# Optimization experiments

Measured on AMD Instinct MI355X. Metric: run time of the kernel, lower is better.

The kernel has to match this reference:

```python
import jax, jax.numpy as jnp
import numpy as np

HEADS = 8
DIM_HEAD = 64
QUERY_DIM = 512
CONTEXT_DIM = 768
INNER = HEADS * DIM_HEAD  # 512
SCALE = DIM_HEAD ** -0.5


def setup_inputs() -> dict:
    key = jax.random.key(0)
    ks = jax.random.split(key, 7)
    B, N, M = 4, 2048, 2048
    x = jax.random.normal(ks[0], (B, N, QUERY_DIM), dtype=jnp.float32)
    context = jax.random.normal(ks[1], (B, M, CONTEXT_DIM), dtype=jnp.float32)
    # torch Linear weights: [out_features, in_features], y = x @ W.T
    s = 0.02
    Wq = jax.random.normal(ks[2], (INNER, QUERY_DIM), dtype=jnp.float32) * s
    Wk = jax.random.normal(ks[3], (INNER, CONTEXT_DIM), dtype=jnp.float32) * s
    Wv = jax.random.normal(ks[4], (INNER, CONTEXT_DIM), dtype=jnp.float32) * s
    Wo = jax.random.normal(ks[5], (QUERY_DIM, INNER), dtype=jnp.float32) * s
    bo = jax.random.normal(ks[6], (QUERY_DIM,), dtype=jnp.float32) * s
    return {"x": x, "context": context, "Wq": Wq, "Wk": Wk, "Wv": Wv, "Wo": Wo, "bo": bo}


def reference(x, context, Wq, Wk, Wv, Wo, bo):
    b, n, _ = x.shape
    m = context.shape[1]
    h, d = HEADS, DIM_HEAD
    # Projections (bias=False for q/k/v)
    q = jnp.einsum('bnc,ec->bne', x, Wq)        # [b, n, inner]
    k = jnp.einsum('bmc,ec->bme', context, Wk)  # [b, m, inner]
    v = jnp.einsum('bmc,ec->bme', context, Wv)
    # Split heads
    q = q.reshape(b, n, h, d)
    k = k.reshape(b, m, h, d)
    v = v.reshape(b, m, h, d)
    # Scores in fp32 (original casts q,k to float), scaled by dim_head**-0.5
    sim = jnp.einsum('bihd,bjhd->bhij', q.astype(jnp.float32), k.astype(jnp.float32)) * SCALE
    attn = jax.nn.softmax(sim, axis=-1).astype(v.dtype)
    out = jnp.einsum('bhij,bjhd->bihd', attn, v).reshape(b, n, h * d)
    # Output projection with bias (dropout=0 -> identity)
    return jnp.einsum('bne,oe->bno', out, Wo) + bo
```

## Files before the change

kernel.cpp:

```cpp
#include <hip/hip_runtime.h>
#include <hip/hip_bf16.h>
#include <math.h>


typedef __bf16 bf16x8 __attribute__((ext_vector_type(8)));
typedef __bf16 bf16x4 __attribute__((ext_vector_type(4)));
typedef float f32x4 __attribute__((ext_vector_type(4)));

#define QSCALE 0.18033688011112042f

#if __has_builtin(__builtin_amdgcn_exp2f)
#define EXP2(x) __builtin_amdgcn_exp2f(x)
#else
#define EXP2(x) exp2f(x)
#endif

__device__ __forceinline__ f32x4 mfma32(bf16x8 a, bf16x8 b, f32x4 c) {
  return __builtin_amdgcn_mfma_f32_16x16x32_bf16(a, b, c, 0, 0, 0);
}

__global__ __launch_bounds__(256) void cast_all(
    const float* __restrict__ x, const float* __restrict__ ctx,
    const float* __restrict__ wq, const float* __restrict__ wk,
    const float* __restrict__ wv, const float* __restrict__ wo,
    __bf16* __restrict__ xb, __bf16* __restrict__ cb,
    __bf16* __restrict__ wqb, __bf16* __restrict__ wkb,
    __bf16* __restrict__ wvb, __bf16* __restrict__ wob) {
  const int B0 = 1048576;
  const int B1 = 2621440;
  const int B2 = 2686976;
  const int B3 = 2785280;
  const int B4 = 2883584;
  const int B5 = 2949120;
  for (int i = blockIdx.x * blockDim.x + threadIdx.x; i < B5;
       i += gridDim.x * blockDim.x) {
    const float* s;
    __bf16* d;
    int off;
    if (i < B0)      { s = x;   d = xb;  off = i; }
    else if (i < B1) { s = ctx; d = cb;  off = i - B0; }
    else if (i < B2) { s = wq;  d = wqb; off = i - B1; }
    else if (i < B3) { s = wk;  d = wkb; off = i - B2; }
    else if (i < B4) { s = wv;  d = wvb; off = i - B3; }
    else             { s = wo;  d = wob; off = i - B4; }
    float4 f = ((const float4*)s)[off];
    union { __bf16 b[4]; ushort4 u; } cv;
    cv.b[0] = (__bf16)f.x; cv.b[1] = (__bf16)f.y;
    cv.b[2] = (__bf16)f.z; cv.b[3] = (__bf16)f.w;
    ((ushort4*)d)[off] = cv.u;
  }
}

template <int MODE>
__device__ __forceinline__ void gemm_body(
    const __bf16* __restrict__ A, const __bf16* __restrict__ W,
    __bf16* __restrict__ Cout, int Kd, float scale, int m0, int n0,
    __bf16 (*As)[72], __bf16 (*Bs)[72]) {
  const int t = threadIdx.x;
  const int w = t >> 6;
  const int lane = t & 63;
  const int ln = lane & 15;
  const int qd = lane >> 4;
  const int wm = (w >> 1) * 64;
  const int wn = (w & 1) * 64;

  f32x4 zero4 = {0.f, 0.f, 0.f, 0.f};
  f32x4 acc[4][4];
#pragma unroll
  for (int i = 0; i < 4; ++i)
#pragma unroll
    for (int j = 0; j < 4; ++j) acc[i][j] = zero4;

  const int r0 = t >> 2;
  const int c0 = (t & 3) * 16;
  const __bf16* gA0 = A + (size_t)(m0 + r0) * Kd + c0;
  const __bf16* gA1 = A + (size_t)(m0 + r0 + 64) * Kd + c0;
  const __bf16* gB0 = W + (size_t)(n0 + r0) * Kd + c0;
  const __bf16* gB1 = W + (size_t)(n0 + r0 + 64) * Kd + c0;

  uint4 a00 = *(const uint4*)gA0, a01 = *(const uint4*)(gA0 + 8);
  uint4 a10 = *(const uint4*)gA1, a11 = *(const uint4*)(gA1 + 8);
  uint4 b00 = *(const uint4*)gB0, b01 = *(const uint4*)(gB0 + 8);
  uint4 b10 = *(const uint4*)gB1, b11 = *(const uint4*)(gB1 + 8);

  for (int kc = 0; kc < Kd; kc += 64) {
    __syncthreads();
    *(uint4*)&As[r0][c0] = a00;       *(uint4*)&As[r0][c0 + 8] = a01;
    *(uint4*)&As[r0 + 64][c0] = a10;  *(uint4*)&As[r0 + 64][c0 + 8] = a11;
    *(uint4*)&Bs[r0][c0] = b00;       *(uint4*)&Bs[r0][c0 + 8] = b01;
    *(uint4*)&Bs[r0 + 64][c0] = b10;  *(uint4*)&Bs[r0 + 64][c0 + 8] = b11;
    __syncthreads();
    if (kc + 64 < Kd) {
      a00 = *(const uint4*)(gA0 + kc + 64);
      a01 = *(const uint4*)(gA0 + kc + 72);
      a10 = *(const uint4*)(gA1 + kc + 64);
      a11 = *(const uint4*)(gA1 + kc + 72);
      b00 = *(const uint4*)(gB0 + kc + 64);
      b01 = *(const uint4*)(gB0 + kc + 72);
      b10 = *(const uint4*)(gB1 + kc + 64);
      b11 = *(const uint4*)(gB1 + kc + 72);
    }
#pragma unroll
    for (int kst = 0; kst < 2; ++kst) {
      bf16x8 af[4], bfr[4];
#pragma unroll
      for (int i = 0; i < 4; ++i) {
        af[i] = *(const bf16x8*)&As[wm + i * 16 + ln][kst * 32 + qd * 8];
        bfr[i] = *(const bf16x8*)&Bs[wn + i * 16 + ln][kst * 32 + qd * 8];
      }
#pragma unroll
      for (int i = 0; i < 4; ++i)
#pragma unroll
        for (int j = 0; j < 4; ++j) {
          if (MODE == 1)
            acc[i][j] = mfma32(af[i], bfr[j], acc[i][j]);
          else
            acc[i][j] = mfma32(bfr[j], af[i], acc[i][j]);
        }
    }
  }

#pragma unroll
  for (int i = 0; i < 4; ++i)
#pragma unroll
    for (int j = 0; j < 4; ++j) {
      if (MODE == 0) {
        const int gm = m0 + wm + i * 16 + ln;
        const int gn0 = n0 + wn + j * 16 + qd * 4;
        const int bb = gm >> 11, tok = gm & 2047;
        const int hh = gn0 >> 6, dd0 = gn0 & 63;
        bf16x4 v;
#pragma unroll
        for (int rg = 0; rg < 4; ++rg) v[rg] = (__bf16)(acc[i][j][rg] * scale);
        *(bf16x4*)(Cout + (((size_t)bb * 8 + hh) * 2048 + tok) * 64 + dd0) = v;
      } else {
        const int gm0 = m0 + wm + i * 16 + qd * 4;
        const int gn = n0 + wn + j * 16 + ln;
        const int bb = gm0 >> 11, tok0 = gm0 & 2047;
        const int hh = gn >> 6, dd = gn & 63;
        bf16x4 v;
#pragma unroll
        for (int rg = 0; rg < 4; ++rg) v[rg] = (__bf16)acc[i][j][rg];
        *(bf16x4*)(Cout + (((size_t)bb * 8 + hh) * 64 + dd) * 2048 + tok0) = v;
      }
    }
}

__global__ __launch_bounds__(256, 3) void proj_qkv(
    const __bf16* __restrict__ xb, const __bf16* __restrict__ cb,
    const __bf16* __restrict__ Wq, const __bf16* __restrict__ Wk,
    const __bf16* __restrict__ Wv, __bf16* __restrict__ Qw,
    __bf16* __restrict__ Kw, __bf16* __restrict__ Vtw) {
  __shared__ __align__(16) __bf16 As[128][72];
  __shared__ __align__(16) __bf16 Bs[128][72];
  const int m0 = blockIdx.x * 128;
  const int job = blockIdx.y >> 2;
  const int n0 = (blockIdx.y & 3) * 128;
  if (job == 0)
    gemm_body<0>(xb, Wq, Qw, 512, QSCALE, m0, n0, As, Bs);
  else if (job == 1)
    gemm_body<0>(cb, Wk, Kw, 768, 1.0f, m0, n0, As, Bs);
  else
    gemm_body<1>(cb, Wv, Vtw, 768, 1.0f, m0, n0, As, Bs);
}

__global__ __launch_bounds__(256) void gemm_out(
    const __bf16* __restrict__ O0, const __bf16* __restrict__ O1,
    const float* __restrict__ lbuf,
    const __bf16* __restrict__ B,
    float* __restrict__ C, const float* __restrict__ bias) {
  const int m0 = blockIdx.x * 64;
  const int n0 = blockIdx.y * 128;
  const int t = threadIdx.x;
  const int w = t >> 6;
  const int lane = t & 63;
  const int ln = lane & 15;
  const int qd = lane >> 4;
  const int wm = (w >> 1) * 32;
  const int wn = (w & 1) * 64;

  __shared__ __align__(16) __bf16 As[64][72];
  __shared__ __align__(16) __bf16 Bs[128][72];

  f32x4 zero4 = {0.f, 0.f, 0.f, 0.f};
  f32x4 acc[2][4];
#pragma unroll
  for (int i = 0; i < 2; ++i)
#pragma unroll
    for (int j = 0; j < 4; ++j) acc[i][j] = zero4;

  const int r0 = t >> 2;
  const int c0 = (t & 3) * 16;
  const int gm_s = m0 + r0;
  const int bidx = gm_s >> 11, tok_s = gm_s & 2047;
  const size_t aoff = (size_t)gm_s * 512 + c0;
  const __bf16* gB0 = B + (size_t)(n0 + r0) * 512 + c0;
  const __bf16* gB1 = B + (size_t)(n0 + r0 + 64) * 512 + c0;

  float inv[8];
#pragma unroll
  for (int hh = 0; hh < 8; ++hh) {
    const float l0 = lbuf[((size_t)bidx * 8 + hh) * 2048 + tok_s];
    const float l1 = lbuf[65536 + ((size_t)bidx * 8 + hh) * 2048 + tok_s];
    inv[hh] = 1.0f / (l0 + l1);
  }

  uint4 o00 = *(const uint4*)(O0 + aoff), o01 = *(const uint4*)(O0 + aoff + 8);
  uint4 o10 = *(const uint4*)(O1 + aoff), o11 = *(const uint4*)(O1 + aoff + 8);
  uint4 b00 = *(const uint4*)gB0, b01 = *(const uint4*)(gB0 + 8);
  uint4 b10 = *(const uint4*)gB1, b11 = *(const uint4*)(gB1 + 8);

  for (int kc = 0; kc < 512; kc += 64) {
    const float iv = inv[kc >> 6];
    union { bf16x8 v; uint4 u; } u0, u1, r0v, r1v;
    u0.u = o00; u1.u = o10;
#pragma unroll
    for (int e = 0; e < 8; ++e)
      r0v.v[e] = (__bf16)(((float)u0.v[e] + (float)u1.v[e]) * iv);
    u0.u = o01; u1.u = o11;
#pragma unroll
    for (int e = 0; e < 8; ++e)
      r1v.v[e] = (__bf16)(((float)u0.v[e] + (float)u1.v[e]) * iv);
    __syncthreads();
    *(uint4*)&As[r0][c0] = r0v.u;
    *(uint4*)&As[r0][c0 + 8] = r1v.u;
    *(uint4*)&Bs[r0][c0] = b00;       *(uint4*)&Bs[r0][c0 + 8] = b01;
    *(uint4*)&Bs[r0 + 64][c0] = b10;  *(uint4*)&Bs[r0 + 64][c0 + 8] = b11;
    __syncthreads();
    if (kc + 64 < 512) {
      o00 = *(const uint4*)(O0 + aoff + kc + 64);
      o01 = *(const uint4*)(O0 + aoff + kc + 72);
      o10 = *(const uint4*)(O1 + aoff + kc + 64);
      o11 = *(const uint4*)(O1 + aoff + kc + 72);
      b00 = *(const uint4*)(gB0 + kc + 64);
      b01 = *(const uint4*)(gB0 + kc + 72);
      b10 = *(const uint4*)(gB1 + kc + 64);
      b11 = *(const uint4*)(gB1 + kc + 72);
    }
#pragma unroll
    for (int kst = 0; kst < 2; ++kst) {
      bf16x8 af[2], bfr[4];
#pragma unroll
      for (int i = 0; i < 2; ++i)
        af[i] = *(const bf16x8*)&As[wm + i * 16 + ln][kst * 32 + qd * 8];
#pragma unroll
      for (int j = 0; j < 4; ++j)
        bfr[j] = *(const bf16x8*)&Bs[wn + j * 16 + ln][kst * 32 + qd * 8];
#pragma unroll
      for (int i = 0; i < 2; ++i)
#pragma unroll
        for (int j = 0; j < 4; ++j)
          acc[i][j] = mfma32(bfr[j], af[i], acc[i][j]);
    }
  }

#pragma unroll
  for (int i = 0; i < 2; ++i)
#pragma unroll
    for (int j = 0; j < 4; ++j) {
      const int gm = m0 + wm + i * 16 + ln;
      const int gn0 = n0 + wn + j * 16 + qd * 4;
      f32x4 bi = *(const f32x4*)&bias[gn0];
      f32x4 v = acc[i][j] + bi;
      *(f32x4*)&C[(size_t)gm * 512 + gn0] = v;
    }
}

__global__ __launch_bounds__(256, 4) void attn_kernel(
    const __bf16* __restrict__ Q,
    const __bf16* __restrict__ K,
    const __bf16* __restrict__ Vt,
    __bf16* __restrict__ Oh,
    float* __restrict__ lbuf) {
  const int S = 2048;
  const int qt = blockIdx.x;
  const int bh = blockIdx.y;
  const int sp = blockIdx.z;
  const int b = bh >> 3, h = bh & 7;
  const int t = threadIdx.x;
  const int w = t >> 6;
  const int lane = t & 63;
  const int ln = lane & 15;
  const int qd = lane >> 4;

  __shared__ __align__(16) __bf16 Ks[128][72];
  __shared__ __align__(16) __bf16 Vs[64][136];

  bf16x8 bq[2][2];
  {
    const __bf16* qb =
        Q + ((size_t)bh * S + qt * 128 + w * 32 + ln) * 64 + qd * 8;
#pragma unroll
    for (int mt = 0; mt < 2; ++mt)
#pragma unroll
      for (int kst = 0; kst < 2; ++kst)
        bq[mt][kst] = *(const bf16x8*)(qb + mt * 1024 + kst * 32);
  }

  f32x4 zero4 = {0.f, 0.f, 0.f, 0.f};
  f32x4 o[2][4];
  f32x4 o_l[2];
#pragma unroll
  for (int mt = 0; mt < 2; ++mt) {
#pragma unroll
    for (int i = 0; i < 4; ++i) o[mt][i] = zero4;
    o_l[mt] = zero4;
  }
  bf16x8 ones8;
  {
    union { unsigned short u[8]; bf16x8 v; } U;
#pragma unroll
    for (int e = 0; e < 8; ++e) U.u[e] = 0x3F80;
    ones8 = U.v;
  }

  const int kr = t >> 1, kc = (t & 1) * 32;
  const int krow =
      (kr & ~31) | ((kr & 4) << 2) | (((kr >> 3) & 3) << 2) | (kr & 3);
  const int vd = t >> 2, cV = t & 3;
  const int kt0 = sp * 8;

  for (int kt = kt0; kt < kt0 + 8; ++kt) {
    const uint4* gK =
        (const uint4*)(K + ((size_t)bh * S + kt * 128 + kr) * 64 + kc);
    const uint4* gV =
        (const uint4*)(Vt + ((size_t)bh * 64 + vd) * S + kt * 128 + cV * 32);
    uint4 kv0 = gK[0], kv1 = gK[1], kv2 = gK[2], kv3 = gK[3];
    uint4 vv0 = gV[0], vv1 = gV[1], vv2 = gV[2], vv3 = gV[3];
    __syncthreads();
    {
      uint4* dK = (uint4*)&Ks[krow][kc];
      dK[0] = kv0; dK[1] = kv1; dK[2] = kv2; dK[3] = kv3;
      uint4* dV = (uint4*)&Vs[vd][cV * 32];
      dV[0] = vv0; dV[1] = vv1; dV[2] = vv2; dV[3] = vv3;
    }
    __syncthreads();

#pragma unroll
    for (int c = 0; c < 4; ++c) {
      f32x4 s[2][2];
      s[0][0] = zero4; s[0][1] = zero4; s[1][0] = zero4; s[1][1] = zero4;
#pragma unroll
      for (int e = 0; e < 2; ++e) {
        const int nt = c * 2 + e;
#pragma unroll
        for (int kst = 0; kst < 2; ++kst) {
          bf16x8 ak = *(const bf16x8*)&Ks[nt * 16 + ln][kst * 32 + qd * 8];
          s[e][0] = mfma32(ak, bq[0][kst], s[e][0]);
          s[e][1] = mfma32(ak, bq[1][kst], s[e][1]);
        }
      }
#pragma unroll
      for (int e = 0; e < 2; ++e)
#pragma unroll
        for (int mt = 0; mt < 2; ++mt)
#pragma unroll
          for (int rg = 0; rg < 4; ++rg) s[e][mt][rg] = EXP2(s[e][mt][rg]);
      bf16x8 p[2];
#pragma unroll
      for (int mt = 0; mt < 2; ++mt) {
#pragma unroll
        for (int rg = 0; rg < 4; ++rg) {
          p[mt][rg] = (__bf16)s[0][mt][rg];
          p[mt][rg + 4] = (__bf16)s[1][mt][rg];
        }
      }
      o_l[0] = mfma32(ones8, p[0], o_l[0]);
      o_l[1] = mfma32(ones8, p[1], o_l[1]);
#pragma unroll
      for (int i = 0; i < 4; ++i) {
        bf16x8 av = *(const bf16x8*)&Vs[i * 16 + ln][c * 32 + qd * 8];
        o[0][i] = mfma32(av, p[0], o[0][i]);
        o[1][i] = mfma32(av, p[1], o[1][i]);
      }
    }
  }

  __bf16* Osp = Oh + (size_t)sp * 8192 * 512;
#pragma unroll
  for (int mt = 0; mt < 2; ++mt) {
    const int tok = qt * 128 + w * 32 + mt * 16 + ln;
    if (qd == 0) lbuf[((size_t)sp * 32 + bh) * 2048 + tok] = o_l[mt][0];
#pragma unroll
    for (int i = 0; i < 4; ++i) {
      bf16x4 v;
#pragma unroll
      for (int rg = 0; rg < 4; ++rg) v[rg] = (__bf16)o[mt][i][rg];
      const int col = h * 64 + i * 16 + qd * 4;
      *(bf16x4*)&Osp[((size_t)b * S + tok) * 512 + col] = v;
    }
  }
}

extern "C" void kernel_launch(void* const* d_in, const int* in_sizes, int n_in,
                              void* d_out, int out_size, void* d_ws,
                              size_t ws_size, hipStream_t stream) {
  const float* x = (const float*)d_in[0];
  const float* ctx = (const float*)d_in[1];
  const float* Wq = (const float*)d_in[2];
  const float* Wk = (const float*)d_in[3];
  const float* Wv = (const float*)d_in[4];
  const float* Wo = (const float*)d_in[5];
  const float* bo = (const float*)d_in[6];

  char* p = (char*)d_ws;
  __bf16* xb = (__bf16*)p;   p += (size_t)8192 * 512 * 2;
  __bf16* cb = (__bf16*)p;   p += (size_t)8192 * 768 * 2;
  __bf16* wqb = (__bf16*)p;  p += (size_t)512 * 512 * 2;
  __bf16* wkb = (__bf16*)p;  p += (size_t)512 * 768 * 2;
  __bf16* wvb = (__bf16*)p;  p += (size_t)512 * 768 * 2;
  __bf16* wob = (__bf16*)p;  p += (size_t)512 * 512 * 2;
  __bf16* Qw = (__bf16*)p;   p += (size_t)8192 * 512 * 2;
  __bf16* Kw = (__bf16*)p;   p += (size_t)8192 * 512 * 2;
  __bf16* Vtw = (__bf16*)p;  p += (size_t)8192 * 512 * 2;
  __bf16* Oh = (__bf16*)p;   p += (size_t)2 * 8192 * 512 * 2;
  float* lbuf = (float*)p;   p += (size_t)2 * 32 * 2048 * 4;

  cast_all<<<2880, 256, 0, stream>>>(x, ctx, Wq, Wk, Wv, Wo, xb, cb, wqb, wkb,
                                     wvb, wob);

  dim3 gp(64, 12);
  proj_qkv<<<gp, 256, 0, stream>>>(xb, cb, wqb, wkb, wvb, Qw, Kw, Vtw);

  dim3 ga(16, 32, 2);
  attn_kernel<<<ga, 256, 0, stream>>>(Qw, Kw, Vtw, Oh, lbuf);

  dim3 go(128, 4);
  gemm_out<<<go, 256, 0, stream>>>(Oh, Oh + (size_t)8192 * 512, lbuf, wob,
                                   (float*)d_out, bo);
}
```

Before: 175.0 us.

## Fuse activation fp32-to-bf16 cast into projection GEMM loads and prefetch K/V tiles

Removes the separate cast of x and context to bf16 and instead converts fp32 activations to bf16 while loading GEMM tiles in proj_qkv, leaving only a small weight-cast kernel. This avoids writing and re-reading the bf16 activation copies. The attention kernel now software-pipelines K/V global loads so the next tile is fetched before the current tile's compute. The cost is more register pressure and twice the global read bytes per A tile in the projection, plus repeated conversion work across the N-tile blocks.

```diff
diff --git a/kernel.cpp b/kernel.cpp
--- a/kernel.cpp
+++ b/kernel.cpp
@@ -19,30 +19,39 @@
   return __builtin_amdgcn_mfma_f32_16x16x32_bf16(a, b, c, 0, 0, 0);
 }
 
-__global__ __launch_bounds__(256) void cast_all(
-    const float* __restrict__ x, const float* __restrict__ ctx,
+__device__ __forceinline__ void ld16f(const float* p, uint4& o0, uint4& o1) {
+  float4 f0 = ((const float4*)p)[0], f1 = ((const float4*)p)[1];
+  float4 f2 = ((const float4*)p)[2], f3 = ((const float4*)p)[3];
+  union { __bf16 h[16]; uint4 u[2]; } c;
+  c.h[0] = (__bf16)f0.x; c.h[1] = (__bf16)f0.y;
+  c.h[2] = (__bf16)f0.z; c.h[3] = (__bf16)f0.w;
+  c.h[4] = (__bf16)f1.x; c.h[5] = (__bf16)f1.y;
+  c.h[6] = (__bf16)f1.z; c.h[7] = (__bf16)f1.w;
+  c.h[8] = (__bf16)f2.x; c.h[9] = (__bf16)f2.y;
+  c.h[10] = (__bf16)f2.z; c.h[11] = (__bf16)f2.w;
+  c.h[12] = (__bf16)f3.x; c.h[13] = (__bf16)f3.y;
+  c.h[14] = (__bf16)f3.z; c.h[15] = (__bf16)f3.w;
+  o0 = c.u[0]; o1 = c.u[1];
+}
+
+__global__ __launch_bounds__(256) void cast_w(
     const float* __restrict__ wq, const float* __restrict__ wk,
     const float* __restrict__ wv, const float* __restrict__ wo,
-    __bf16* __restrict__ xb, __bf16* __restrict__ cb,
     __bf16* __restrict__ wqb, __bf16* __restrict__ wkb,
     __bf16* __restrict__ wvb, __bf16* __restrict__ wob) {
-  const int B0 = 1048576;
-  const int B1 = 2621440;
-  const int B2 = 2686976;
-  const int B3 = 2785280;
-  const int B4 = 2883584;
-  const int B5 = 2949120;
-  for (int i = blockIdx.x * blockDim.x + threadIdx.x; i < B5;
+  const int B0 = 65536;
+  const int B1 = 163840;
+  const int B2 = 262144;
+  const int B3 = 327680;
+  for (int i = blockIdx.x * blockDim.x + threadIdx.x; i < B3;
        i += gridDim.x * blockDim.x) {
     const float* s;
     __bf16* d;
     int off;
-    if (i < B0)      { s = x;   d = xb;  off = i; }
-    else if (i < B1) { s = ctx; d = cb;  off = i - B0; }
-    else if (i < B2) { s = wq;  d = wqb; off = i - B1; }
-    else if (i < B3) { s = wk;  d = wkb; off = i - B2; }
-    else if (i < B4) { s = wv;  d = wvb; off = i - B3; }
-    else             { s = wo;  d = wob; off = i - B4; }
+    if (i < B0)      { s = wq; d = wqb; off = i; }
+    else if (i < B1) { s = wk; d = wkb; off = i - B0; }
+    else if (i < B2) { s = wv; d = wvb; off = i - B1; }
+    else             { s = wo; d = wob; off = i - B2; }
     float4 f = ((const float4*)s)[off];
     union { __bf16 b[4]; ushort4 u; } cv;
     cv.b[0] = (__bf16)f.x; cv.b[1] = (__bf16)f.y;
@@ -53,7 +62,7 @@
 
 template <int MODE>
 __device__ __forceinline__ void gemm_body(
-    const __bf16* __restrict__ A, const __bf16* __restrict__ W,
+    const float* __restrict__ A, const __bf16* __restrict__ W,
     __bf16* __restrict__ Cout, int Kd, float scale, int m0, int n0,
     __bf16 (*As)[72], __bf16 (*Bs)[72]) {
   const int t = threadIdx.x;
@@ -73,13 +82,14 @@
 
   const int r0 = t >> 2;
   const int c0 = (t & 3) * 16;
-  const __bf16* gA0 = A + (size_t)(m0 + r0) * Kd + c0;
-  const __bf16* gA1 = A + (size_t)(m0 + r0 + 64) * Kd + c0;
+  const float* gA0 = A + (size_t)(m0 + r0) * Kd + c0;
+  const float* gA1 = A + (size_t)(m0 + r0 + 64) * Kd + c0;
   const __bf16* gB0 = W + (size_t)(n0 + r0) * Kd + c0;
   const __bf16* gB1 = W + (size_t)(n0 + r0 + 64) * Kd + c0;
 
-  uint4 a00 = *(const uint4*)gA0, a01 = *(const uint4*)(gA0 + 8);
-  uint4 a10 = *(const uint4*)gA1, a11 = *(const uint4*)(gA1 + 8);
+  uint4 a00, a01, a10, a11;
+  ld16f(gA0, a00, a01);
+  ld16f(gA1, a10, a11);
   uint4 b00 = *(const uint4*)gB0, b01 = *(const uint4*)(gB0 + 8);
   uint4 b10 = *(const uint4*)gB1, b11 = *(const uint4*)(gB1 + 8);
 
@@ -91,10 +101,8 @@
     *(uint4*)&Bs[r0 + 64][c0] = b10;  *(uint4*)&Bs[r0 + 64][c0 + 8] = b11;
     __syncthreads();
     if (kc + 64 < Kd) {
-      a00 = *(const uint4*)(gA0 + kc + 64);
-      a01 = *(const uint4*)(gA0 + kc + 72);
-      a10 = *(const uint4*)(gA1 + kc + 64);
-      a11 = *(const uint4*)(gA1 + kc + 72);
+      ld16f(gA0 + kc + 64, a00, a01);
+      ld16f(gA1 + kc + 64, a10, a11);
       b00 = *(const uint4*)(gB0 + kc + 64);
       b01 = *(const uint4*)(gB0 + kc + 72);
       b10 = *(const uint4*)(gB1 + kc + 64);
@@ -147,7 +155,7 @@
 }
 
 __global__ __launch_bounds__(256, 3) void proj_qkv(
-    const __bf16* __restrict__ xb, const __bf16* __restrict__ cb,
+    const float* __restrict__ x, const float* __restrict__ ctx,
     const __bf16* __restrict__ Wq, const __bf16* __restrict__ Wk,
     const __bf16* __restrict__ Wv, __bf16* __restrict__ Qw,
     __bf16* __restrict__ Kw, __bf16* __restrict__ Vtw) {
@@ -157,11 +165,11 @@
   const int job = blockIdx.y >> 2;
   const int n0 = (blockIdx.y & 3) * 128;
   if (job == 0)
-    gemm_body<0>(xb, Wq, Qw, 512, QSCALE, m0, n0, As, Bs);
+    gemm_body<0>(x, Wq, Qw, 512, QSCALE, m0, n0, As, Bs);
   else if (job == 1)
-    gemm_body<0>(cb, Wk, Kw, 768, 1.0f, m0, n0, As, Bs);
+    gemm_body<0>(ctx, Wk, Kw, 768, 1.0f, m0, n0, As, Bs);
   else
-    gemm_body<1>(cb, Wv, Vtw, 768, 1.0f, m0, n0, As, Bs);
+    gemm_body<1>(ctx, Wv, Vtw, 768, 1.0f, m0, n0, As, Bs);
 }
 
 __global__ __launch_bounds__(256) void gemm_out(
@@ -320,13 +328,18 @@
   const int vd = t >> 2, cV = t & 3;
   const int kt0 = sp * 8;
 
+  const __bf16* gKbase = K + ((size_t)bh * S + kr) * 64 + kc;
+  const __bf16* gVbase = Vt + ((size_t)bh * 64 + vd) * S + cV * 32;
+
+  uint4 kv0, kv1, kv2, kv3, vv0, vv1, vv2, vv3;
+  {
+    const uint4* gK = (const uint4*)(gKbase + (size_t)kt0 * 128 * 64);
+    const uint4* gV = (const uint4*)(gVbase + kt0 * 128);
+    kv0 = gK[0]; kv1 = gK[1]; kv2 = gK[2]; kv3 = gK[3];
+    vv0 = gV[0]; vv1 = gV[1]; vv2 = gV[2]; vv3 = gV[3];
+  }
+
   for (int kt = kt0; kt < kt0 + 8; ++kt) {
-    const uint4* gK =
-        (const uint4*)(K + ((size_t)bh * S + kt * 128 + kr) * 64 + kc);
-    const uint4* gV =
-        (const uint4*)(Vt + ((size_t)bh * 64 + vd) * S + kt * 128 + cV * 32);
-    uint4 kv0 = gK[0], kv1 = gK[1], kv2 = gK[2], kv3 = gK[3];
-    uint4 vv0 = gV[0], vv1 = gV[1], vv2 = gV[2], vv3 = gV[3];
     __syncthreads();
     {
       uint4* dK = (uint4*)&Ks[krow][kc];
@@ -335,6 +348,12 @@
       dV[0] = vv0; dV[1] = vv1; dV[2] = vv2; dV[3] = vv3;
     }
     __syncthreads();
+    if (kt + 1 < kt0 + 8) {
+      const uint4* gK = (const uint4*)(gKbase + (size_t)(kt + 1) * 128 * 64);
+      const uint4* gV = (const uint4*)(gVbase + (kt + 1) * 128);
+      kv0 = gK[0]; kv1 = gK[1]; kv2 = gK[2]; kv3 = gK[3];
+      vv0 = gV[0]; vv1 = gV[1]; vv2 = gV[2]; vv3 = gV[3];
+    }
 
 #pragma unroll
     for (int c = 0; c < 4; ++c) {
@@ -404,8 +423,6 @@
   const float* bo = (const float*)d_in[6];
 
   char* p = (char*)d_ws;
-  __bf16* xb = (__bf16*)p;   p += (size_t)8192 * 512 * 2;
-  __bf16* cb = (__bf16*)p;   p += (size_t)8192 * 768 * 2;
   __bf16* wqb = (__bf16*)p;  p += (size_t)512 * 512 * 2;
   __bf16* wkb = (__bf16*)p;  p += (size_t)512 * 768 * 2;
   __bf16* wvb = (__bf16*)p;  p += (size_t)512 * 768 * 2;
@@ -416,11 +433,10 @@
   __bf16* Oh = (__bf16*)p;   p += (size_t)2 * 8192 * 512 * 2;
   float* lbuf = (float*)p;   p += (size_t)2 * 32 * 2048 * 4;
 
-  cast_all<<<2880, 256, 0, stream>>>(x, ctx, Wq, Wk, Wv, Wo, xb, cb, wqb, wkb,
-                                     wvb, wob);
+  cast_w<<<320, 256, 0, stream>>>(Wq, Wk, Wv, Wo, wqb, wkb, wvb, wob);
 
   dim3 gp(64, 12);
-  proj_qkv<<<gp, 256, 0, stream>>>(xb, cb, wqb, wkb, wvb, Qw, Kw, Vtw);
+  proj_qkv<<<gp, 256, 0, stream>>>(x, ctx, wqb, wkb, wvb, Qw, Kw, Vtw);
 
   dim3 ga(16, 32, 2);
   attn_kernel<<<ga, 256, 0, stream>>>(Qw, Kw, Vtw, Oh, lbuf);
```

New measurement: 185.1 us. 5.7% more time.
